# Kernel tuning notes

Measured on AMD Instinct MI355X. Metric: run time of the kernel, lower is better.

The kernel has to match this reference:

```python
import jax, jax.numpy as jnp
import numpy as np

D_MODEL = 1024
NUM_HEADS = 16
HEAD_DIM = D_MODEL // NUM_HEADS
ROPE_BASE = 10000.0


def setup_inputs() -> dict:
    key = jax.random.key(0)
    ks = jax.random.split(key, 9)
    B, S = 2, 2048
    x = jax.random.normal(ks[0], (B, S, D_MODEL), dtype=jnp.float32)
    s = 1.0 / np.sqrt(D_MODEL)
    Wq = jax.random.normal(ks[1], (D_MODEL, D_MODEL), dtype=jnp.float32) * s
    bq = jnp.zeros((D_MODEL,), dtype=jnp.float32)
    Wk = jax.random.normal(ks[2], (D_MODEL, D_MODEL), dtype=jnp.float32) * s
    bk = jnp.zeros((D_MODEL,), dtype=jnp.float32)
    Wv = jax.random.normal(ks[3], (D_MODEL, D_MODEL), dtype=jnp.float32) * s
    bv = jnp.zeros((D_MODEL,), dtype=jnp.float32)
    Wo = jax.random.normal(ks[4], (D_MODEL, D_MODEL), dtype=jnp.float32) * s
    bo = jnp.zeros((D_MODEL,), dtype=jnp.float32)
    return {"x": x, "Wq": Wq, "bq": bq, "Wk": Wk, "bk": bk,
            "Wv": Wv, "bv": bv, "Wo": Wo, "bo": bo}


def _apply_rope(x):
    # x: [B, H, S, Dh]; interleaved complex-pair RoPE (torch.view_as_complex style)
    B, H, S, Dh = x.shape
    inv_freq = 1.0 / (ROPE_BASE ** (jnp.arange(0, Dh, 2, dtype=jnp.float32) / Dh))
    pos = jnp.arange(S, dtype=jnp.float32)
    freqs = pos[:, None] * inv_freq[None, :]            # [S, Dh/2]
    cos, sin = jnp.cos(freqs), jnp.sin(freqs)           # each [S, Dh/2]
    x2 = x.reshape(B, H, S, Dh // 2, 2)
    xr, xi = x2[..., 0], x2[..., 1]
    out_r = xr * cos - xi * sin
    out_i = xr * sin + xi * cos
    return jnp.stack([out_r, out_i], axis=-1).reshape(B, H, S, Dh)


def reference(x, Wq, bq, Wk, bk, Wv, bv, Wo, bo):
    B, S, _ = x.shape
    H, Dh = NUM_HEADS, HEAD_DIM
    def proj(W, b):
        y = jnp.einsum('bsd,ed->bse', x, W) + b          # torch Linear: x @ W.T + b
        return y.reshape(B, S, H, Dh).transpose(0, 2, 1, 3)  # [B,H,S,Dh]
    Q = _apply_rope(proj(Wq, bq))
    K = _apply_rope(proj(Wk, bk))
    V = proj(Wv, bv)
    scale = 1.0 / jnp.sqrt(jnp.float32(Dh))
    scores = jnp.einsum('bhqd,bhkd->bhqk', Q, K) * scale
    causal = jnp.tril(jnp.ones((S, S), dtype=bool))
    scores = jnp.where(causal, scores, jnp.float32(-jnp.inf))
    attn = jax.nn.softmax(scores, axis=-1)
    out = jnp.einsum('bhqk,bhkd->bhqd', attn, V)         # [B,H,S,Dh]
    out = out.transpose(0, 2, 1, 3).reshape(B, S, H * Dh)
    return jnp.einsum('bsd,ed->bse', out, Wo) + bo
```

## Files before the change

### kernel.cpp

```cpp
#include <hip/hip_runtime.h>
#include <stdint.h>

#define S_LEN 2048
#define BATCH 2
#define DM 1024
#define NH 16
#define DH 64
#define MROWS 4096

typedef unsigned short u16;
typedef unsigned int u32;
typedef __attribute__((ext_vector_type(8))) short bf16x8;
typedef __attribute__((ext_vector_type(4))) float f32x4;
typedef __attribute__((ext_vector_type(2))) unsigned u32x2;

union pack8 { u32 w[4]; bf16x8 v8; };

__device__ inline u16 f2bf(float f) {
  union { float f; unsigned u; } v; v.f = f;
  unsigned u = v.u;
  unsigned r = u + 0x7fffu + ((u >> 16) & 1u);
  return (u16)(r >> 16);
}

__device__ inline u32 pkbf(float lo, float hi) {
  u32 r;
  asm("v_cvt_pk_bf16_f32 %0, %1, %2" : "=v"(r) : "v"(lo), "v"(hi));
  return r;
}

__device__ inline float bf2f(short s) {
  union { u32 u; float f; } c; c.u = ((u32)(u16)s) << 16;
  return c.f;
}

__device__ __forceinline__ void gload_lds16(const u16* g, u16* l) {
  __builtin_amdgcn_global_load_lds(
      (const __attribute__((address_space(1))) u32*)g,
      (__attribute__((address_space(3))) u32*)l, 16, 0, 0);
}

__global__ void convert_k(const float* __restrict__ x, const float* __restrict__ wq,
                          const float* __restrict__ wk, const float* __restrict__ wv,
                          const float* __restrict__ wo, u16* __restrict__ xb,
                          u16* __restrict__ wb) {
  int i = blockIdx.x * blockDim.x + threadIdx.x;
  const int total = (MROWS * DM + 4 * DM * DM) / 4;
  if (i >= total) return;
  int e = i * 4;
  const float* src;
  u16* dst;
  if (e < MROWS * DM) {
    src = x + e; dst = xb + e;
  } else {
    int j = e - MROWS * DM;
    int w = j >> 20;
    int o = j & ((1 << 20) - 1);
    src = (w == 0) ? wq + o : (w == 1) ? wk + o : (w == 2) ? wv + o : wo + o;
    dst = wb + j;
  }
  float4 v = *(const float4*)src;
  uint2 r;
  r.x = (unsigned)f2bf(v.x) | ((unsigned)f2bf(v.y) << 16);
  r.y = (unsigned)f2bf(v.z) | ((unsigned)f2bf(v.w) << 16);
  *(uint2*)dst = r;
}

__global__ void rope_k(float2* __restrict__ tab, float* __restrict__ kmax) {
  int i = blockIdx.x * blockDim.x + threadIdx.x;
  if (i < 32) kmax[i] = 0.f;
  if (i >= S_LEN * 32) return;
  int s = i >> 5, p = i & 31;
  float inv = expf(-(float)p * 0.28782313662425575f);
  float a = (float)s * inv;
  tab[i] = make_float2(cosf(a), sinf(a));
}

__global__ void knorm_k(const u16* __restrict__ K, float* __restrict__ kmax) {
  const int row = blockIdx.x * 256 + threadIdx.x;
  const int bh = row >> 11;
  const u16* p = K + (size_t)row * DH;
  float ss = 0.f;
#pragma unroll
  for (int i = 0; i < 8; i++) {
    bf16x8 v = *(const bf16x8*)(p + i * 8);
#pragma unroll
    for (int j = 0; j < 8; j++) { float f = bf2f(v[j]); ss += f * f; }
  }
  float kn = sqrtf(ss);
#pragma unroll
  for (int d = 1; d < 64; d <<= 1) kn = fmaxf(kn, __shfl_xor(kn, d));
  if ((threadIdx.x & 63) == 0)
    atomicMax((unsigned*)(kmax + bh), __float_as_uint(kn));
}

__launch_bounds__(256)
__global__ void gemm_k(const u16* __restrict__ A,
                       const u16* __restrict__ w0, const u16* __restrict__ w1,
                       const u16* __restrict__ w2,
                       const float* __restrict__ b0, const float* __restrict__ b1,
                       const float* __restrict__ b2,
                       const float2* __restrict__ rope,
                       void* __restrict__ o0, void* __restrict__ o1, void* __restrict__ o2,
                       int mode0) {
  const int mode = mode0 + (int)(blockIdx.x >> 8);
  const int tile = blockIdx.x & 255;
  const int mt = tile >> 3, nt = tile & 7;
  const int mbase = mt * 128, nbase = nt * 128;
  const u16* W = (mode == 1) ? w1 : (mode == 2) ? w2 : w0;
  const float* bias = (mode == 1) ? b1 : (mode == 2) ? b2 : b0;
  void* outp = (mode == 1) ? o1 : (mode == 2) ? o2 : o0;

  __shared__ u16 As[128 * 32];
  __shared__ u16 Bs[128 * 32];

  const int t = threadIdx.x;
  const int lane = t & 63, wvi = t >> 6;
  const int lr = lane & 15, lg = lane >> 4;
  const int wm = (wvi >> 1) * 64, wn = (wvi & 1) * 64;

  f32x4 acc[4][4] = {};
  const int srow = t >> 2;
  const int scol = (t & 3) * 8;

  for (int kk = 0; kk < DM; kk += 32) {
    gload_lds16(A + (size_t)(mbase + srow) * DM + kk + scol, &As[wvi * 512]);
    gload_lds16(A + (size_t)(mbase + 64 + srow) * DM + kk + scol, &As[2048 + wvi * 512]);
    gload_lds16(W + (size_t)(nbase + srow) * DM + kk + scol, &Bs[wvi * 512]);
    gload_lds16(W + (size_t)(nbase + 64 + srow) * DM + kk + scol, &Bs[2048 + wvi * 512]);
    __syncthreads();

    bf16x8 af[4], bfr[4];
#pragma unroll
    for (int mi = 0; mi < 4; mi++)
      af[mi] = *(const bf16x8*)&As[(wm + mi * 16 + lr) * 32 + lg * 8];
#pragma unroll
    for (int ni = 0; ni < 4; ni++)
      bfr[ni] = *(const bf16x8*)&Bs[(wn + ni * 16 + lr) * 32 + lg * 8];
#pragma unroll
    for (int mi = 0; mi < 4; mi++)
#pragma unroll
      for (int ni = 0; ni < 4; ni++)
        acc[mi][ni] = __builtin_amdgcn_mfma_f32_16x16x32_bf16(af[mi], bfr[ni], acc[mi][ni], 0, 0, 0);
    __syncthreads();
  }

#pragma unroll
  for (int ni = 0; ni < 4; ni++) {
    const int col = nbase + wn + ni * 16 + lr;
    const float bv = bias[col];
#pragma unroll
    for (int mi = 0; mi < 4; mi++) {
      const int row0 = mbase + wm + mi * 16 + lg * 4;
      f32x4 v = acc[mi][ni];
#pragma unroll
      for (int r = 0; r < 4; r++) {
        float val = v[r] + bv;
        const int row = row0 + r;
        if (mode <= 1) {
          float nb = __shfl_xor(val, 1);
          const int d = col & 63, p = d >> 1, s = row & (S_LEN - 1);
          float2 cs = rope[s * 32 + p];
          float ov = (d & 1) ? (nb * cs.y + val * cs.x) : (val * cs.x - nb * cs.y);
          if (mode == 0) ov *= 0.18033688011112042f;
          const int b = row >> 11, h = col >> 6;
          ((u16*)outp)[((size_t)(b * NH + h) * S_LEN + s) * DH + d] = f2bf(ov);
        } else if (mode == 2) {
          const int b = row >> 11, h = col >> 6, d = col & 63, s = row & (S_LEN - 1);
          const int j = s & 31;
          const int pos = (s & ~31) + (((j & 15) >> 2) << 3) + ((j >> 4) << 2) + (j & 3);
          ((u16*)outp)[((size_t)(b * NH + h) * DH + d) * S_LEN + pos] = f2bf(val);
        } else {
          ((float*)outp)[(size_t)row * DM + col] = val;
        }
      }
    }
  }
}

__device__ __forceinline__ void sm_pv(const float a[8], float m, float& l,
                                      bf16x8 v0, bf16x8 v1, bf16x8 v2, bf16x8 v3,
                                      f32x4* o) {
  float p[8];
#pragma unroll
  for (int r = 0; r < 8; r++) p[r] = __builtin_amdgcn_exp2f(a[r] - m);
  l += ((p[0] + p[1]) + (p[2] + p[3])) + ((p[4] + p[5]) + (p[6] + p[7]));
  pack8 pu;
  pu.w[0] = pkbf(p[0], p[1]);
  pu.w[1] = pkbf(p[2], p[3]);
  pu.w[2] = pkbf(p[4], p[5]);
  pu.w[3] = pkbf(p[6], p[7]);
  o[0] = __builtin_amdgcn_mfma_f32_16x16x32_bf16(v0, pu.v8, o[0], 0, 0, 0);
  o[1] = __builtin_amdgcn_mfma_f32_16x16x32_bf16(v1, pu.v8, o[1], 0, 0, 0);
  o[2] = __builtin_amdgcn_mfma_f32_16x16x32_bf16(v2, pu.v8, o[2], 0, 0, 0);
  o[3] = __builtin_amdgcn_mfma_f32_16x16x32_bf16(v3, pu.v8, o[3], 0, 0, 0);
}

__launch_bounds__(256)
__global__ void attn_k(const u16* __restrict__ Q, const u16* __restrict__ K,
                       const u16* __restrict__ Vt, u16* __restrict__ Oo,
                       const float* __restrict__ kmax) {
  const int bh = blockIdx.x & 31;
  const int g = 15 - (int)(blockIdx.x >> 5);
  const int tid = threadIdx.x;
  const int w = tid >> 6;
  const int lane = tid & 63;
  const int lr = lane & 15, lg = lane >> 4;
  const int tile = g * 4 + w;
  const int qbase = tile * 32;
  const int nst = g * 4 + 4;

  __shared__ u16 Ks[2][2048];
  __shared__ u16 Vs[2][2048];

  const u16* Kg = K + (size_t)bh * S_LEN * DH;
  const u16* Vg = Vt + (size_t)bh * DH * S_LEN;

  const int kr = tid >> 3, kcB = (tid & 7) << 4;
  const int vr = tid >> 2, vcB = (tid & 3) << 4;
  const int ksrcoff = ((kcB ^ ((kr & 7) << 4)) >> 1);
  const int vsrcoff = ((vcB ^ (((vr >> 1) & 3) << 4)) >> 1);

  const size_t qoff = ((size_t)bh * S_LEN + qbase + lr) * DH + lg * 8;
  const bf16x8 qA0 = *(const bf16x8*)(Q + qoff);
  const bf16x8 qA1 = *(const bf16x8*)(Q + qoff + 32);
  const bf16x8 qB0 = *(const bf16x8*)(Q + qoff + 16 * DH);
  const bf16x8 qB1 = *(const bf16x8*)(Q + qoff + 16 * DH + 32);

  float ssA = 0.f, ssB = 0.f;
#pragma unroll
  for (int j = 0; j < 8; j++) {
    float a0 = bf2f(qA0[j]), a1 = bf2f(qA1[j]);
    float b0 = bf2f(qB0[j]), b1 = bf2f(qB1[j]);
    ssA += a0 * a0 + a1 * a1;
    ssB += b0 * b0 + b1 * b1;
  }
  ssA += __shfl_xor(ssA, 16); ssA += __shfl_xor(ssA, 32);
  ssB += __shfl_xor(ssB, 16); ssB += __shfl_xor(ssB, 32);
  const float kmx = kmax[bh];
  const float mA = sqrtf(ssA) * kmx;
  const float mB = sqrtf(ssB) * kmx;

  f32x4 oA[4] = {}, oB[4] = {};
  float lA = 0.f, lB = 0.f;
  const f32x4 zero = {};

  const int kmsk = (lr & 7) << 4;
  const int k00 = lr * 64 + (((lg << 4)) ^ kmsk) / 2;
  const int k01 = lr * 64 + ((64 + (lg << 4)) ^ kmsk) / 2;
  const int k10 = (16 + lr) * 64 + (((lg << 4)) ^ kmsk) / 2;
  const int k11 = (16 + lr) * 64 + ((64 + (lg << 4)) ^ kmsk) / 2;
  const int vmsk = ((lr >> 1) & 3) << 4;
  const int vo = ((lg << 4) ^ vmsk) / 2;

  gload_lds16(Kg + (size_t)kr * DH + ksrcoff, &Ks[0][w << 9]);
  gload_lds16(Vg + (size_t)vr * S_LEN + vsrcoff, &Vs[0][w << 9]);

  for (int s = 0; s < nst; ++s) {
    const int b = s & 1;
    if (s + 1 < nst) {
      gload_lds16(Kg + (size_t)((s + 1) * 32 + kr) * DH + ksrcoff, &Ks[b ^ 1][w << 9]);
      gload_lds16(Vg + (size_t)vr * S_LEN + (s + 1) * 32 + vsrcoff, &Vs[b ^ 1][w << 9]);
    }
    __syncthreads();

    const u16* Kb = Ks[b];
    const u16* Vb = Vs[b];
    bf16x8 kc0 = *(const bf16x8*)&Kb[k00];
    bf16x8 kc1 = *(const bf16x8*)&Kb[k01];
    bf16x8 kc2 = *(const bf16x8*)&Kb[k10];
    bf16x8 kc3 = *(const bf16x8*)&Kb[k11];
    bf16x8 v0 = *(const bf16x8*)&Vb[(lr) * 32 + vo];
    bf16x8 v1 = *(const bf16x8*)&Vb[(16 + lr) * 32 + vo];
    bf16x8 v2 = *(const bf16x8*)&Vb[(32 + lr) * 32 + vo];
    bf16x8 v3 = *(const bf16x8*)&Vb[(48 + lr) * 32 + vo];

    f32x4 s0A = __builtin_amdgcn_mfma_f32_16x16x32_bf16(kc0, qA0, zero, 0, 0, 0);
    s0A = __builtin_amdgcn_mfma_f32_16x16x32_bf16(kc1, qA1, s0A, 0, 0, 0);
    f32x4 s1A = __builtin_amdgcn_mfma_f32_16x16x32_bf16(kc2, qA0, zero, 0, 0, 0);
    s1A = __builtin_amdgcn_mfma_f32_16x16x32_bf16(kc3, qA1, s1A, 0, 0, 0);
    f32x4 s0B = __builtin_amdgcn_mfma_f32_16x16x32_bf16(kc0, qB0, zero, 0, 0, 0);
    s0B = __builtin_amdgcn_mfma_f32_16x16x32_bf16(kc1, qB1, s0B, 0, 0, 0);
    f32x4 s1B = __builtin_amdgcn_mfma_f32_16x16x32_bf16(kc2, qB0, zero, 0, 0, 0);
    s1B = __builtin_amdgcn_mfma_f32_16x16x32_bf16(kc3, qB1, s1B, 0, 0, 0);

    const int qrelA = qbase + lr - (s << 5) - (lg << 2);
    const int qrelB = qrelA + 16;
    float aA[8], aB[8];
#pragma unroll
    for (int r = 0; r < 4; r++) {
      aA[r]     = (r <= qrelA)      ? s0A[r] : -__builtin_inff();
      aA[4 + r] = (r + 16 <= qrelA) ? s1A[r] : -__builtin_inff();
      aB[r]     = (r <= qrelB)      ? s0B[r] : -__builtin_inff();
      aB[4 + r] = (r + 16 <= qrelB) ? s1B[r] : -__builtin_inff();
    }
    sm_pv(aA, mA, lA, v0, v1, v2, v3, oA);
    sm_pv(aB, mB, lB, v0, v1, v2, v3, oB);

    __syncthreads();
  }

  lA += __shfl_xor(lA, 16); lA += __shfl_xor(lA, 32);
  lB += __shfl_xor(lB, 16); lB += __shfl_xor(lB, 32);
  const float rlA = __builtin_amdgcn_rcpf(lA);
  const float rlB = __builtin_amdgcn_rcpf(lB);

  const int bb = bh >> 4, h = bh & 15;
  const size_t obaseA = ((size_t)bb * S_LEN + qbase + lr) * DM + h * DH;
  const size_t obaseB = obaseA + (size_t)16 * DM;
#pragma unroll
  for (int dt = 0; dt < 4; dt++) {
    u32x2 pkA, pkB;
    pkA.x = pkbf(oA[dt][0] * rlA, oA[dt][1] * rlA);
    pkA.y = pkbf(oA[dt][2] * rlA, oA[dt][3] * rlA);
    pkB.x = pkbf(oB[dt][0] * rlB, oB[dt][1] * rlB);
    pkB.y = pkbf(oB[dt][2] * rlB, oB[dt][3] * rlB);
    *(u32x2*)(Oo + obaseA + dt * 16 + lg * 4) = pkA;
    *(u32x2*)(Oo + obaseB + dt * 16 + lg * 4) = pkB;
  }
}

extern "C" void kernel_launch(void* const* d_in, const int* in_sizes, int n_in,
                              void* d_out, int out_size, void* d_ws, size_t ws_size,
                              hipStream_t stream) {
  const float* x  = (const float*)d_in[0];
  const float* Wq = (const float*)d_in[1];
  const float* bq = (const float*)d_in[2];
  const float* Wk = (const float*)d_in[3];
  const float* bk = (const float*)d_in[4];
  const float* Wv = (const float*)d_in[5];
  const float* bv = (const float*)d_in[6];
  const float* Wo = (const float*)d_in[7];
  const float* bo = (const float*)d_in[8];

  char* ws = (char*)d_ws;
  u16* xb    = (u16*)(ws);
  u16* wb    = (u16*)(ws + (8u << 20));
  u16* Qb    = (u16*)(ws + (16u << 20));
  u16* Kb    = (u16*)(ws + (24u << 20));
  u16* Vtb   = (u16*)(ws + (32u << 20));
  u16* AOb   = (u16*)(ws + (40u << 20));
  float2* rt = (float2*)(ws + (48u << 20));
  float* kmx = (float*)(ws + (48u << 20) + (512u << 10));

  convert_k<<<8192, 256, 0, stream>>>(x, Wq, Wk, Wv, Wo, xb, wb);
  rope_k<<<256, 256, 0, stream>>>(rt, kmx);
  gemm_k<<<768, 256, 0, stream>>>(xb, wb, wb + (1u << 20), wb + (2u << 20),
                                  bq, bk, bv, rt, Qb, Kb, Vtb, 0);
  knorm_k<<<256, 256, 0, stream>>>(Kb, kmx);
  attn_k<<<512, 256, 0, stream>>>(Qb, Kb, Vtb, AOb, kmx);
  gemm_k<<<256, 256, 0, stream>>>(AOb, wb + (3u << 20), wb + (3u << 20), wb + (3u << 20),
                                  bo, bo, bo, rt, d_out, d_out, d_out, 3);
}
```

Before: 153.9 us.

## Double-buffer GEMM LDS tiles and use partial vmcnt waits in attention loop

The projection GEMM now keeps two LDS buffers for the A and W tiles and prefetches the next k-slice while the current one feeds MFMA. Both the GEMM and the attention loop replace __syncthreads with explicit s_waitcnt vmcnt(N) plus s_barrier, so only the older loads must land before compute. Previously every global load was fully drained each iteration. This aims to overlap global-to-LDS transfers with MFMA work, at the cost of doubled shared memory in the GEMM and correctness that depends on exact vmcnt counts.

```diff
diff --git a/kernel.cpp b/kernel.cpp
--- a/kernel.cpp
+++ b/kernel.cpp
@@ -111,8 +111,8 @@
   const float* bias = (mode == 1) ? b1 : (mode == 2) ? b2 : b0;
   void* outp = (mode == 1) ? o1 : (mode == 2) ? o2 : o0;
 
-  __shared__ u16 As[128 * 32];
-  __shared__ u16 Bs[128 * 32];
+  __shared__ u16 As[2][128 * 32];
+  __shared__ u16 Bs[2][128 * 32];
 
   const int t = threadIdx.x;
   const int lane = t & 63, wvi = t >> 6;
@@ -123,26 +123,39 @@
   const int srow = t >> 2;
   const int scol = (t & 3) * 8;
 
+  gload_lds16(A + (size_t)(mbase + srow) * DM + scol, &As[0][wvi * 512]);
+  gload_lds16(A + (size_t)(mbase + 64 + srow) * DM + scol, &As[0][2048 + wvi * 512]);
+  gload_lds16(W + (size_t)(nbase + srow) * DM + scol, &Bs[0][wvi * 512]);
+  gload_lds16(W + (size_t)(nbase + 64 + srow) * DM + scol, &Bs[0][2048 + wvi * 512]);
+
   for (int kk = 0; kk < DM; kk += 32) {
-    gload_lds16(A + (size_t)(mbase + srow) * DM + kk + scol, &As[wvi * 512]);
-    gload_lds16(A + (size_t)(mbase + 64 + srow) * DM + kk + scol, &As[2048 + wvi * 512]);
-    gload_lds16(W + (size_t)(nbase + srow) * DM + kk + scol, &Bs[wvi * 512]);
-    gload_lds16(W + (size_t)(nbase + 64 + srow) * DM + kk + scol, &Bs[2048 + wvi * 512]);
-    __syncthreads();
+    const int b = (kk >> 5) & 1;
+    if (kk + 32 < DM) {
+      gload_lds16(A + (size_t)(mbase + srow) * DM + kk + 32 + scol, &As[b ^ 1][wvi * 512]);
+      gload_lds16(A + (size_t)(mbase + 64 + srow) * DM + kk + 32 + scol, &As[b ^ 1][2048 + wvi * 512]);
+      gload_lds16(W + (size_t)(nbase + srow) * DM + kk + 32 + scol, &Bs[b ^ 1][wvi * 512]);
+      gload_lds16(W + (size_t)(nbase + 64 + srow) * DM + kk + 32 + scol, &Bs[b ^ 1][2048 + wvi * 512]);
+      asm volatile("s_waitcnt vmcnt(4)" ::: "memory");
+    } else {
+      asm volatile("s_waitcnt vmcnt(0)" ::: "memory");
+    }
+    __builtin_amdgcn_s_barrier();
 
     bf16x8 af[4], bfr[4];
 #pragma unroll
     for (int mi = 0; mi < 4; mi++)
-      af[mi] = *(const bf16x8*)&As[(wm + mi * 16 + lr) * 32 + lg * 8];
+      af[mi] = *(const bf16x8*)&As[b][(wm + mi * 16 + lr) * 32 + lg * 8];
 #pragma unroll
     for (int ni = 0; ni < 4; ni++)
-      bfr[ni] = *(const bf16x8*)&Bs[(wn + ni * 16 + lr) * 32 + lg * 8];
+      bfr[ni] = *(const bf16x8*)&Bs[b][(wn + ni * 16 + lr) * 32 + lg * 8];
 #pragma unroll
     for (int mi = 0; mi < 4; mi++)
 #pragma unroll
       for (int ni = 0; ni < 4; ni++)
         acc[mi][ni] = __builtin_amdgcn_mfma_f32_16x16x32_bf16(af[mi], bfr[ni], acc[mi][ni], 0, 0, 0);
-    __syncthreads();
+
+    __builtin_amdgcn_s_barrier();
+    asm volatile("" ::: "memory");
   }
 
 #pragma unroll
@@ -261,8 +274,11 @@
     if (s + 1 < nst) {
       gload_lds16(Kg + (size_t)((s + 1) * 32 + kr) * DH + ksrcoff, &Ks[b ^ 1][w << 9]);
       gload_lds16(Vg + (size_t)vr * S_LEN + (s + 1) * 32 + vsrcoff, &Vs[b ^ 1][w << 9]);
+      asm volatile("s_waitcnt vmcnt(2)" ::: "memory");
+    } else {
+      asm volatile("s_waitcnt vmcnt(0)" ::: "memory");
     }
-    __syncthreads();
+    __builtin_amdgcn_s_barrier();
 
     const u16* Kb = Ks[b];
     const u16* Vb = Vs[b];
@@ -297,7 +313,8 @@
     sm_pv(aA, mA, lA, v0, v1, v2, v3, oA);
     sm_pv(aB, mB, lB, v0, v1, v2, v3, oB);
 
-    __syncthreads();
+    __builtin_amdgcn_s_barrier();
+    asm volatile("" ::: "memory");
   }
 
   lA += __shfl_xor(lA, 16); lA += __shfl_xor(lA, 32);
```

After: 178.0 us. +15.7%, slower.

## Run attention as single-wave blocks with per-wave K/V staging, no barriers

Applied to the files above, without the earlier changes.

The attention kernel changes from 256-thread blocks, where four waves share K/V tiles in LDS, to 64-thread blocks where each wave owns one 32-row query tile. Each wave stages its own K/V tiles with four async global-to-LDS loads per tensor and uses s_waitcnt vmcnt instead of __syncthreads. Each tile now iterates only up to its own causal bound rather than the group's bound. The aim is to remove block-level barriers and the wasted causal stages, at the cost of four times more K/V traffic from L2 and a launch order that schedules the light tiles first.

```diff
diff --git a/kernel.cpp b/kernel.cpp
--- a/kernel.cpp
+++ b/kernel.cpp
@@ -196,19 +196,16 @@
   o[3] = __builtin_amdgcn_mfma_f32_16x16x32_bf16(v3, pu.v8, o[3], 0, 0, 0);
 }
 
-__launch_bounds__(256)
+__launch_bounds__(64)
 __global__ void attn_k(const u16* __restrict__ Q, const u16* __restrict__ K,
                        const u16* __restrict__ Vt, u16* __restrict__ Oo,
                        const float* __restrict__ kmax) {
   const int bh = blockIdx.x & 31;
-  const int g = 15 - (int)(blockIdx.x >> 5);
-  const int tid = threadIdx.x;
-  const int w = tid >> 6;
-  const int lane = tid & 63;
+  const int tile = (int)(blockIdx.x >> 5);
+  const int qbase = tile * 32;
+  const int nst = tile + 1;
+  const int lane = threadIdx.x;
   const int lr = lane & 15, lg = lane >> 4;
-  const int tile = g * 4 + w;
-  const int qbase = tile * 32;
-  const int nst = g * 4 + 4;
 
   __shared__ u16 Ks[2][2048];
   __shared__ u16 Vs[2][2048];
@@ -216,10 +213,10 @@
   const u16* Kg = K + (size_t)bh * S_LEN * DH;
   const u16* Vg = Vt + (size_t)bh * DH * S_LEN;
 
-  const int kr = tid >> 3, kcB = (tid & 7) << 4;
-  const int vr = tid >> 2, vcB = (tid & 3) << 4;
-  const int ksrcoff = ((kcB ^ ((kr & 7) << 4)) >> 1);
-  const int vsrcoff = ((vcB ^ (((vr >> 1) & 3) << 4)) >> 1);
+  const int krow = lane >> 3;
+  const int ksoff = ((((lane & 7) << 4) ^ ((lane >> 3) << 4)) >> 1);
+  const int vrow = lane >> 2;
+  const int vsoff = ((((lane & 3) << 4) ^ (((lane >> 3) & 3) << 4)) >> 1);
 
   const size_t qoff = ((size_t)bh * S_LEN + qbase + lr) * DH + lg * 8;
   const bf16x8 qA0 = *(const bf16x8*)(Q + qoff);
@@ -253,16 +250,28 @@
   const int vmsk = ((lr >> 1) & 3) << 4;
   const int vo = ((lg << 4) ^ vmsk) / 2;
 
-  gload_lds16(Kg + (size_t)kr * DH + ksrcoff, &Ks[0][w << 9]);
-  gload_lds16(Vg + (size_t)vr * S_LEN + vsrcoff, &Vs[0][w << 9]);
+#define STAGE(s32, bb)                                                          \
+  {                                                                             \
+    const u16* kgs = Kg + (size_t)(s32) * DH;                                   \
+    const u16* vgs = Vg + (s32);                                                \
+    _Pragma("unroll")                                                           \
+    for (int i = 0; i < 4; i++)                                                 \
+      gload_lds16(kgs + (size_t)(i * 8 + krow) * DH + ksoff, &Ks[bb][i * 512]); \
+    _Pragma("unroll")                                                           \
+    for (int i = 0; i < 4; i++)                                                 \
+      gload_lds16(vgs + (size_t)(i * 16 + vrow) * S_LEN + vsoff, &Vs[bb][i * 512]); \
+  }
+
+  STAGE(0, 0);
 
   for (int s = 0; s < nst; ++s) {
     const int b = s & 1;
     if (s + 1 < nst) {
-      gload_lds16(Kg + (size_t)((s + 1) * 32 + kr) * DH + ksrcoff, &Ks[b ^ 1][w << 9]);
-      gload_lds16(Vg + (size_t)vr * S_LEN + (s + 1) * 32 + vsrcoff, &Vs[b ^ 1][w << 9]);
+      STAGE((s + 1) * 32, b ^ 1);
+      asm volatile("s_waitcnt vmcnt(8)" ::: "memory");
+    } else {
+      asm volatile("s_waitcnt vmcnt(0)" ::: "memory");
     }
-    __syncthreads();
 
     const u16* Kb = Ks[b];
     const u16* Vb = Vs[b];
@@ -296,9 +305,8 @@
     }
     sm_pv(aA, mA, lA, v0, v1, v2, v3, oA);
     sm_pv(aB, mB, lB, v0, v1, v2, v3, oB);
-
-    __syncthreads();
-  }
+  }
+#undef STAGE
 
   lA += __shfl_xor(lA, 16); lA += __shfl_xor(lA, 32);
   lB += __shfl_xor(lB, 16); lB += __shfl_xor(lB, 32);
@@ -348,7 +356,7 @@
   gemm_k<<<768, 256, 0, stream>>>(xb, wb, wb + (1u << 20), wb + (2u << 20),
                                   bq, bk, bv, rt, Qb, Kb, Vtb, 0);
   knorm_k<<<256, 256, 0, stream>>>(Kb, kmx);
-  attn_k<<<512, 256, 0, stream>>>(Qb, Kb, Vtb, AOb, kmx);
+  attn_k<<<2048, 64, 0, stream>>>(Qb, Kb, Vtb, AOb, kmx);
   gemm_k<<<256, 256, 0, stream>>>(AOb, wb + (3u << 20), wb + (3u << 20), wb + (3u << 20),
                                   bo, bo, bo, rt, d_out, d_out, d_out, 3);
 }
```

Result: faster. 150.7 us (-2.0%).
